# Kernel tuning notes

Hardware: AMD Instinct MI355X
Metric: run time of the kernel (lower is better)

## Reference

```python
import jax, jax.numpy as jnp
import numpy as np

B, L, D = 8192, 2048, 256


def setup_inputs() -> dict:
    key = jax.random.key(0)
    kx, kl = jax.random.split(key)
    x = jax.random.normal(kx, (B, D), dtype=jnp.float32)
    landmarks = jax.random.normal(kl, (L, D), dtype=jnp.float32)
    return {"x": x, "landmarks": landmarks}


def reference(x, landmarks):
    # RBF layer: out[b, l] = exp(-gamma * sum_d (landmarks[l, d] - x[b, d])^2)
    # gamma='auto' -> 1 / n_features (landmarks.shape[1])
    gamma = jnp.float32(1.0 / landmarks.shape[1])
    # avoids materializing the [B, L, D] broadcast-diff intermediate)
    x2 = jnp.sum(x * x, axis=-1, keepdims=True)          # [B, 1]
    l2 = jnp.sum(landmarks * landmarks, axis=-1)         # [L]
    cross = jnp.einsum('bd,ld->bl', x, landmarks)        # [B, L]
    d2 = jnp.maximum(x2 + l2[None, :] - 2.0 * cross, 0.0)
    return jnp.exp(-gamma * d2)
```

## Files before the change

### kernel.cpp

```cpp
#include <hip/hip_runtime.h>


typedef __bf16 bf16x8 __attribute__((ext_vector_type(8)));
typedef float  f32x4  __attribute__((ext_vector_type(4)));

#define B_ROWS 8192
#define L_ROWS 2048
#define K_DIM  256
#define NEG_GAMMA (-1.0f / 256.0f)

#define GLD_LDS(g, l) __builtin_amdgcn_global_load_lds(                      \
    (const __attribute__((address_space(1))) void*)(g),                      \
    (__attribute__((address_space(3))) void*)(l), 16, 0, 0)

__device__ __forceinline__ unsigned short f32_to_bf16_rne(float f) {
    union { float f; unsigned int u; } v; v.f = f;
    unsigned int u = v.u;
    return (unsigned short)((u + 0x7fffu + ((u >> 16) & 1u)) >> 16);
}

__global__ __launch_bounds__(256) void cvt_rows_kernel(
    const float* __restrict__ x, const float* __restrict__ lm,
    unsigned short* __restrict__ xb, unsigned short* __restrict__ lb,
    float* __restrict__ gx2, float* __restrict__ gl2)
{
    const int lane = threadIdx.x & 63;
    const int row  = blockIdx.x * 4 + (threadIdx.x >> 6);
    const float* src; unsigned short* dst; float* nrm;
    if (row < B_ROWS) {
        src = x + (size_t)row * K_DIM; dst = xb + (size_t)row * K_DIM; nrm = gx2 + row;
    } else {
        const int r = row - B_ROWS;
        src = lm + (size_t)r * K_DIM; dst = lb + (size_t)r * K_DIM; nrm = gl2 + r;
    }
    const float4 v = ((const float4*)src)[lane];
    ushort4 o;
    o.x = f32_to_bf16_rne(v.x);
    o.y = f32_to_bf16_rne(v.y);
    o.z = f32_to_bf16_rne(v.z);
    o.w = f32_to_bf16_rne(v.w);
    ((ushort4*)dst)[lane] = o;
    float s = v.x*v.x + v.y*v.y + v.z*v.z + v.w*v.w;
    #pragma unroll
    for (int off = 32; off > 0; off >>= 1) s += __shfl_down(s, off, 64);
    if (lane == 0) nrm[0] = NEG_GAMMA * s;
}

__global__ __launch_bounds__(256) void rbf_gemm_kernel(
    const unsigned short* __restrict__ Lmat,
    const unsigned short* __restrict__ Xmat,
    const float* __restrict__ gl2,
    const float* __restrict__ gx2,
    float* __restrict__ out)
{
    __shared__ unsigned short As[128 * 64];
    __shared__ unsigned short Bs[128 * 64];

    const int tid  = threadIdx.x;
    const int wave = tid >> 6;
    const int lane = tid & 63;
    const int wm = wave >> 1, wn = wave & 1;
    const int bn = blockIdx.x;
    const int bm = blockIdx.y;

    f32x4 acc[4][4];
    #pragma unroll
    for (int i = 0; i < 4; ++i)
        #pragma unroll
        for (int j = 0; j < 4; ++j)
            acc[i][j] = (f32x4){0.f, 0.f, 0.f, 0.f};

    const int lrow = lane >> 3;
    const int lblk = (lane & 7) ^ lrow;

    const unsigned short* Ab = Lmat + (size_t)(bm * 128) * K_DIM;
    const unsigned short* Bb = Xmat + (size_t)(bn * 128) * K_DIM;

    const int rlo = lane & 15;
    const int q   = lane >> 4;

    for (int k0 = 0; k0 < K_DIM; k0 += 64) {
        #pragma unroll
        for (int it = 0; it < 4; ++it) {
            const int r = wave * 32 + it * 8;
            GLD_LDS(Ab + (size_t)(r + lrow) * K_DIM + k0 + lblk * 8, &As[r * 64]);
            GLD_LDS(Bb + (size_t)(r + lrow) * K_DIM + k0 + lblk * 8, &Bs[r * 64]);
        }
        __syncthreads();

        #pragma unroll
        for (int kk = 0; kk < 64; kk += 32) {
            const int kb = (kk >> 3) + q;
            const int pb = (kb ^ (rlo & 7)) * 8;
            bf16x8 af[4], bfr[4];
            #pragma unroll
            for (int t = 0; t < 4; ++t) {
                af[t]  = *(const bf16x8*)&As[(wm*64 + t*16 + rlo) * 64 + pb];
                bfr[t] = *(const bf16x8*)&Bs[(wn*64 + t*16 + rlo) * 64 + pb];
            }
            #pragma unroll
            for (int mt = 0; mt < 4; ++mt)
                #pragma unroll
                for (int nt = 0; nt < 4; ++nt)
                    acc[mt][nt] = __builtin_amdgcn_mfma_f32_16x16x32_bf16(
                        af[mt], bfr[nt], acc[mt][nt], 0, 0, 0);
        }
        __syncthreads();
    }

    const float twog = 2.0f / 256.0f;
    const int b0 = bn * 128 + wn * 64 + rlo;
    const int l0 = bm * 128 + wm * 64 + q * 4;
    #pragma unroll
    for (int nt = 0; nt < 4; ++nt) {
        const int b = b0 + nt * 16;
        const float gx = gx2[b];
        float* orow = out + (size_t)b * L_ROWS;
        #pragma unroll
        for (int mt = 0; mt < 4; ++mt) {
            const int l = l0 + mt * 16;
            const float4 gl = *(const float4*)&gl2[l];
            f32x4 o;
            o[0] = __expf(fminf(fmaf(twog, acc[mt][nt][0], gx + gl.x), 0.f));
            o[1] = __expf(fminf(fmaf(twog, acc[mt][nt][1], gx + gl.y), 0.f));
            o[2] = __expf(fminf(fmaf(twog, acc[mt][nt][2], gx + gl.z), 0.f));
            o[3] = __expf(fminf(fmaf(twog, acc[mt][nt][3], gx + gl.w), 0.f));
            __builtin_nontemporal_store(o, (f32x4*)&orow[l]);
        }
    }
}

extern "C" void kernel_launch(void* const* d_in, const int* in_sizes, int n_in,
                              void* d_out, int out_size, void* d_ws, size_t ws_size,
                              hipStream_t stream) {
    const float* x  = (const float*)d_in[0];
    const float* lm = (const float*)d_in[1];
    float* out = (float*)d_out;

    char* ws = (char*)d_ws;
    unsigned short* xb = (unsigned short*)ws;
    unsigned short* lb = (unsigned short*)(ws + (size_t)B_ROWS*K_DIM*2);
    float* gx2 = (float*)(ws + (size_t)B_ROWS*K_DIM*2 + (size_t)L_ROWS*K_DIM*2);
    float* gl2 = gx2 + B_ROWS;

    cvt_rows_kernel<<<(B_ROWS + L_ROWS)/4, 256, 0, stream>>>(x, lm, xb, lb, gx2, gl2);
    rbf_gemm_kernel<<<dim3(B_ROWS/128, L_ROWS/128), 256, 0, stream>>>(lb, xb, gl2, gx2, out);
}
```

Baseline: 98.11 us.

## Fuse bf16 conversion and row norms into the RBF GEMM kernel

Removes the separate conversion kernel and workspace. The GEMM now loads fp32 tiles of x and landmarks directly, converts them to bf16 in registers and writes them into swizzled LDS, while accumulating per-row squared norms that are reduced through shared memory before the epilogue. This saves a kernel launch and the round trip of the bf16 copies through memory. In exchange, each block rereads fp32 inputs (twice the bytes) and conversion is repeated across blocks. Staging now goes through registers instead of direct global-to-LDS loads, which may add latency because nothing is pipelined.

Result: slower. 102.7 us (+4.6%).

```diff
diff --git a/kernel.cpp b/kernel.cpp
--- a/kernel.cpp
+++ b/kernel.cpp
@@ -9,52 +9,17 @@
 #define K_DIM  256
 #define NEG_GAMMA (-1.0f / 256.0f)
 
-#define GLD_LDS(g, l) __builtin_amdgcn_global_load_lds(                      \
-    (const __attribute__((address_space(1))) void*)(g),                      \
-    (__attribute__((address_space(3))) void*)(l), 16, 0, 0)
-
-__device__ __forceinline__ unsigned short f32_to_bf16_rne(float f) {
-    union { float f; unsigned int u; } v; v.f = f;
-    unsigned int u = v.u;
-    return (unsigned short)((u + 0x7fffu + ((u >> 16) & 1u)) >> 16);
-}
-
-__global__ __launch_bounds__(256) void cvt_rows_kernel(
-    const float* __restrict__ x, const float* __restrict__ lm,
-    unsigned short* __restrict__ xb, unsigned short* __restrict__ lb,
-    float* __restrict__ gx2, float* __restrict__ gl2)
-{
-    const int lane = threadIdx.x & 63;
-    const int row  = blockIdx.x * 4 + (threadIdx.x >> 6);
-    const float* src; unsigned short* dst; float* nrm;
-    if (row < B_ROWS) {
-        src = x + (size_t)row * K_DIM; dst = xb + (size_t)row * K_DIM; nrm = gx2 + row;
-    } else {
-        const int r = row - B_ROWS;
-        src = lm + (size_t)r * K_DIM; dst = lb + (size_t)r * K_DIM; nrm = gl2 + r;
-    }
-    const float4 v = ((const float4*)src)[lane];
-    ushort4 o;
-    o.x = f32_to_bf16_rne(v.x);
-    o.y = f32_to_bf16_rne(v.y);
-    o.z = f32_to_bf16_rne(v.z);
-    o.w = f32_to_bf16_rne(v.w);
-    ((ushort4*)dst)[lane] = o;
-    float s = v.x*v.x + v.y*v.y + v.z*v.z + v.w*v.w;
-    #pragma unroll
-    for (int off = 32; off > 0; off >>= 1) s += __shfl_down(s, off, 64);
-    if (lane == 0) nrm[0] = NEG_GAMMA * s;
-}
-
-__global__ __launch_bounds__(256) void rbf_gemm_kernel(
-    const unsigned short* __restrict__ Lmat,
-    const unsigned short* __restrict__ Xmat,
-    const float* __restrict__ gl2,
-    const float* __restrict__ gx2,
+__global__ __launch_bounds__(256) void rbf_fused_kernel(
+    const float* __restrict__ x,
+    const float* __restrict__ lm,
     float* __restrict__ out)
 {
     __shared__ unsigned short As[128 * 64];
     __shared__ unsigned short Bs[128 * 64];
+    __shared__ float sqA[128][4];
+    __shared__ float sqB[128][4];
+    __shared__ float nA[128];
+    __shared__ float nB[128];
 
     const int tid  = threadIdx.x;
     const int wave = tid >> 6;
@@ -70,22 +35,45 @@
         for (int j = 0; j < 4; ++j)
             acc[i][j] = (f32x4){0.f, 0.f, 0.f, 0.f};
 
-    const int lrow = lane >> 3;
-    const int lblk = (lane & 7) ^ lrow;
+    const int srow = tid >> 2;
+    const int ss   = tid & 3;
 
-    const unsigned short* Ab = Lmat + (size_t)(bm * 128) * K_DIM;
-    const unsigned short* Bb = Xmat + (size_t)(bn * 128) * K_DIM;
+    const float* Ag = lm + (size_t)(bm * 128) * K_DIM;
+    const float* Bg = x  + (size_t)(bn * 128) * K_DIM;
+
+    float aA0 = 0.f, aA1 = 0.f, aB0 = 0.f, aB1 = 0.f;
 
     const int rlo = lane & 15;
     const int q   = lane >> 4;
 
     for (int k0 = 0; k0 < K_DIM; k0 += 64) {
-        #pragma unroll
-        for (int it = 0; it < 4; ++it) {
-            const int r = wave * 32 + it * 8;
-            GLD_LDS(Ab + (size_t)(r + lrow) * K_DIM + k0 + lblk * 8, &As[r * 64]);
-            GLD_LDS(Bb + (size_t)(r + lrow) * K_DIM + k0 + lblk * 8, &Bs[r * 64]);
-        }
+        auto stage = [&](const float* __restrict__ gbase,
+                         unsigned short* __restrict__ sbase,
+                         int row, float& sacc) {
+            const float* g = gbase + (size_t)row * K_DIM + k0 + ss * 16;
+            f32x4 f0 = ((const f32x4*)g)[0];
+            f32x4 f1 = ((const f32x4*)g)[1];
+            f32x4 f2 = ((const f32x4*)g)[2];
+            f32x4 f3 = ((const f32x4*)g)[3];
+            #pragma unroll
+            for (int i = 0; i < 4; ++i) {
+                sacc = fmaf(f0[i], f0[i], sacc);
+                sacc = fmaf(f1[i], f1[i], sacc);
+                sacc = fmaf(f2[i], f2[i], sacc);
+                sacc = fmaf(f3[i], f3[i], sacc);
+            }
+            bf16x8 h0 = __builtin_convertvector(
+                __builtin_shufflevector(f0, f1, 0,1,2,3,4,5,6,7), bf16x8);
+            bf16x8 h1 = __builtin_convertvector(
+                __builtin_shufflevector(f2, f3, 0,1,2,3,4,5,6,7), bf16x8);
+            const int c = row & 7;
+            *(bf16x8*)&sbase[row * 64 + (((2*ss)     ^ c) * 8)] = h0;
+            *(bf16x8*)&sbase[row * 64 + (((2*ss + 1) ^ c) * 8)] = h1;
+        };
+        stage(Ag, As, srow,      aA0);
+        stage(Ag, As, srow + 64, aA1);
+        stage(Bg, Bs, srow,      aB0);
+        stage(Bg, Bs, srow + 64, aB1);
         __syncthreads();
 
         #pragma unroll
@@ -108,24 +96,36 @@
         __syncthreads();
     }
 
+    sqA[srow][ss]      = aA0;
+    sqA[srow + 64][ss] = aA1;
+    sqB[srow][ss]      = aB0;
+    sqB[srow + 64][ss] = aB1;
+    __syncthreads();
+    if (tid < 128) {
+        nA[tid] = NEG_GAMMA * (sqA[tid][0] + sqA[tid][1] + sqA[tid][2] + sqA[tid][3]);
+    } else {
+        const int r = tid - 128;
+        nB[r] = NEG_GAMMA * (sqB[r][0] + sqB[r][1] + sqB[r][2] + sqB[r][3]);
+    }
+    __syncthreads();
+
     const float twog = 2.0f / 256.0f;
-    const int b0 = bn * 128 + wn * 64 + rlo;
-    const int l0 = bm * 128 + wm * 64 + q * 4;
+    const int bt0 = wn * 64 + rlo;
+    const int lt0 = wm * 64 + q * 4;
     #pragma unroll
     for (int nt = 0; nt < 4; ++nt) {
-        const int b = b0 + nt * 16;
-        const float gx = gx2[b];
-        float* orow = out + (size_t)b * L_ROWS;
+        const int bt = bt0 + nt * 16;
+        const float gx = nB[bt];
+        float* orow = out + (size_t)(bn * 128 + bt) * L_ROWS + bm * 128;
         #pragma unroll
         for (int mt = 0; mt < 4; ++mt) {
-            const int l = l0 + mt * 16;
-            const float4 gl = *(const float4*)&gl2[l];
+            const int lt = lt0 + mt * 16;
+            const f32x4 gl = *(const f32x4*)&nA[lt];
             f32x4 o;
-            o[0] = __expf(fminf(fmaf(twog, acc[mt][nt][0], gx + gl.x), 0.f));
-            o[1] = __expf(fminf(fmaf(twog, acc[mt][nt][1], gx + gl.y), 0.f));
-            o[2] = __expf(fminf(fmaf(twog, acc[mt][nt][2], gx + gl.z), 0.f));
-            o[3] = __expf(fminf(fmaf(twog, acc[mt][nt][3], gx + gl.w), 0.f));
-            __builtin_nontemporal_store(o, (f32x4*)&orow[l]);
+            #pragma unroll
+            for (int r = 0; r < 4; ++r)
+                o[r] = __expf(fminf(fmaf(twog, acc[mt][nt][r], gx + gl[r]), 0.f));
+            __builtin_nontemporal_store(o, (f32x4*)&orow[lt]);
         }
     }
 }
@@ -136,13 +136,5 @@
     const float* x  = (const float*)d_in[0];
     const float* lm = (const float*)d_in[1];
     float* out = (float*)d_out;
-
-    char* ws = (char*)d_ws;
-    unsigned short* xb = (unsigned short*)ws;
-    unsigned short* lb = (unsigned short*)(ws + (size_t)B_ROWS*K_DIM*2);
-    float* gx2 = (float*)(ws + (size_t)B_ROWS*K_DIM*2 + (size_t)L_ROWS*K_DIM*2);
-    float* gl2 = gx2 + B_ROWS;
-
-    cvt_rows_kernel<<<(B_ROWS + L_ROWS)/4, 256, 0, stream>>>(x, lm, xb, lb, gx2, gl2);
-    rbf_gemm_kernel<<<dim3(B_ROWS/128, L_ROWS/128), 256, 0, stream>>>(lb, xb, gl2, gx2, out);
+    rbf_fused_kernel<<<dim3(B_ROWS/128, L_ROWS/128), 256, 0, stream>>>(x, lm, out);
 }
```
